# Performance work log

Measured on AMD Instinct MI355X. Metric: run time of the kernel, lower is better.

Reference implementation:

```python
import jax, jax.numpy as jnp
import numpy as np

N_NODES = 50000


def gcn_conv(x, edge_index, W, b, n):
    # PyG GCNConv: xW, add self-loops, symmetric degree normalization,
    # scatter-add messages from source (row) to target (col).
    xw = x @ W
    row, col = edge_index[0], edge_index[1]
    loops = jnp.arange(n, dtype=edge_index.dtype)
    row = jnp.concatenate([row, loops])
    col = jnp.concatenate([col, loops])
    deg = jax.ops.segment_sum(jnp.ones(row.shape[0], dtype=xw.dtype), col, num_segments=n)
    dinv = jnp.where(deg > 0, jax.lax.rsqrt(deg), 0.0)
    norm = dinv[row] * dinv[col]  # [E+N]
    out = jax.ops.segment_sum(xw[row] * norm[:, None], col, num_segments=n)
    return out + b


def setup_inputs() -> dict:
    key = jax.random.key(0)
    ks = jax.random.split(key, 5)
    n, d_in, d_h, d_out, n_edges = N_NODES, 128, 128, 4, 600000
    x = jax.random.normal(ks[0], (n, d_in), dtype=jnp.float32)
    edge_index = jax.random.randint(ks[1], (2, n_edges), 0, n, dtype=jnp.int64)
    W1 = jax.random.normal(ks[2], (d_in, d_h), dtype=jnp.float32) * (1.0 / np.sqrt(d_in))
    b1 = jnp.zeros((d_h,), dtype=jnp.float32)
    W2 = jax.random.normal(ks[3], (d_h, d_h), dtype=jnp.float32) * (1.0 / np.sqrt(d_h))
    b2 = jnp.zeros((d_h,), dtype=jnp.float32)
    Wfc = jax.random.normal(ks[4], (2 * d_h, d_out), dtype=jnp.float32) * (1.0 / np.sqrt(2 * d_h))
    bfc = jnp.zeros((d_out,), dtype=jnp.float32)
    return {"x": x, "edge_index": edge_index, "W1": W1, "b1": b1,
            "W2": W2, "b2": b2, "Wfc": Wfc, "bfc": bfc}


def reference(x, edge_index, W1, b1, W2, b2, Wfc, bfc):
    n = x.shape[0]
    # dropout is identity at inference (training=False)
    h = jax.nn.relu(gcn_conv(x, edge_index, W1, b1, n))
    h = jax.nn.relu(gcn_conv(h, edge_index, W2, b2, n))
    # edge-level gather + concat + linear classifier
    edge_x = jnp.concatenate([h[edge_index[0]], h[edge_index[1]]], axis=-1)  # [E, 2*d_h]
    edge_scores = edge_x @ Wfc + bfc  # [E, d_out]
    return jax.nn.log_softmax(edge_scores, axis=1)
```

## Files before the change

### kernel.cpp

```cpp
#include <hip/hip_runtime.h>
#include <math.h>
#include <stdint.h>

#define D 128
#define SCAN_CHUNK 2048
#define LDA 136

typedef __attribute__((ext_vector_type(8))) short v8s;
typedef __attribute__((ext_vector_type(4))) float v4f;

static __device__ __forceinline__ uint16_t f2bf(float f) {
    uint32_t u = __float_as_uint(f);
    u = (u + 0x7fff + ((u >> 16) & 1)) >> 16;
    return (uint16_t)u;
}
static __device__ __forceinline__ float bf2f(uint16_t h) { return __uint_as_float((uint32_t)h << 16); }
static __device__ __forceinline__ float bf_lo(uint32_t u) { return __uint_as_float(u << 16); }
static __device__ __forceinline__ float bf_hi(uint32_t u) { return __uint_as_float(u & 0xffff0000u); }


__global__ void count_kernel(const int* col, int* cnt, int E) {
    int e = blockIdx.x * blockDim.x + threadIdx.x;
    if (e < E) atomicAdd(&cnt[col[e]], 1);
}

__global__ __launch_bounds__(256) void scanA_kernel(const int* __restrict__ cnt,
                                                    int* __restrict__ bsum, int n) {
    __shared__ int wsum[4];
    int b = blockIdx.x, t = threadIdx.x;
    int base = b * SCAN_CHUNK;
    int s = 0;
#pragma unroll
    for (int k = 0; k < SCAN_CHUNK / 256; k++) {
        int i = base + k * 256 + t;
        if (i < n) s += cnt[i];
    }
#pragma unroll
    for (int off = 32; off > 0; off >>= 1) s += __shfl_xor(s, off, 64);
    if ((t & 63) == 0) wsum[t >> 6] = s;
    __syncthreads();
    if (t == 0) bsum[b] = wsum[0] + wsum[1] + wsum[2] + wsum[3];
}

__global__ __launch_bounds__(64) void scanB_kernel(const int* __restrict__ bsum,
                                                   int* __restrict__ bbase,
                                                   int* __restrict__ offs,
                                                   int nb, int n) {
    int t = threadIdx.x;
    int v = (t < nb) ? bsum[t] : 0;
    int inc = v;
#pragma unroll
    for (int off = 1; off < 64; off <<= 1) {
        int u = __shfl_up(inc, off, 64);
        if (t >= off) inc += u;
    }
    if (t < nb) bbase[t] = inc - v;
    if (t == nb - 1) offs[n] = inc;
}

__global__ __launch_bounds__(256) void scanC_kernel(const int* __restrict__ cnt,
                                                    const int* __restrict__ bbase,
                                                    int* __restrict__ offs,
                                                    float* __restrict__ dinv, int n) {
    __shared__ int stage[SCAN_CHUNK];
    __shared__ int res[SCAN_CHUNK];
    __shared__ int tsum[256];
    int b = blockIdx.x, t = threadIdx.x;
    int base = b * SCAN_CHUNK;
#pragma unroll
    for (int k = 0; k < SCAN_CHUNK / 256; k++) {
        int i = base + k * 256 + t;
        int c = (i < n) ? cnt[i] : 0;
        stage[k * 256 + t] = c;
        if (i < n) dinv[i] = rsqrtf((float)c + 1.0f);
    }
    __syncthreads();
    int my = 0;
#pragma unroll
    for (int j = 0; j < 8; j++) my += stage[t * 8 + j];
    tsum[t] = my;
    __syncthreads();
    for (int off = 1; off < 256; off <<= 1) {
        int v = (t >= off) ? tsum[t - off] : 0;
        __syncthreads();
        tsum[t] += v;
        __syncthreads();
    }
    int run = tsum[t] - my + bbase[b];
#pragma unroll
    for (int j = 0; j < 8; j++) {
        res[t * 8 + j] = run;
        run += stage[t * 8 + j];
    }
    __syncthreads();
#pragma unroll
    for (int k = 0; k < SCAN_CHUNK / 256; k++) {
        int i = base + k * 256 + t;
        if (i < n) offs[i] = res[k * 256 + t];
    }
}

__global__ void fill_kernel(const int* row, const int* col, const int* offs,
                            int* curs, int* adj, int E) {
    int e = blockIdx.x * blockDim.x + threadIdx.x;
    if (e < E) {
        int c = col[e];
        int p = atomicAdd(&curs[c], 1);
        adj[offs[c] + p] = row[e];
    }
}


__global__ __launch_bounds__(256) void packw_kernel(const float* __restrict__ W1,
                                                    const float* __restrict__ W2,
                                                    uint16_t* __restrict__ Wh,
                                                    uint16_t* __restrict__ Wl) {
    int i = blockIdx.x * blockDim.x + threadIdx.x;
    int layer = i >> 14;
    int li = i & 16383;
    int j = li & 7, lane = (li >> 3) & 63, f = li >> 9;
    int kstep = f >> 3, tile = f & 7;
    int k = kstep * 32 + ((lane >> 4) * 8) + j;
    int nn = tile * 16 + (lane & 15);
    const float* W = layer ? W2 : W1;
    float v = W[k * 128 + nn];
    uint16_t h = f2bf(v);
    uint16_t l = f2bf(v - bf2f(h));
    Wh[i] = h;
    Wl[i] = l;
}


__global__ __launch_bounds__(256) void gemm_mfma_kernel(const float* __restrict__ A,
                                                        const uint16_t* __restrict__ Wph,
                                                        const uint16_t* __restrict__ Wpl,
                                                        const float* __restrict__ dinv,
                                                        uint16_t* __restrict__ Cb, int M) {
    __shared__ uint16_t Ah[64][LDA];
    __shared__ uint16_t Al[64][LDA];
    int t = threadIdx.x;
    int base_row = blockIdx.x * 64;

#pragma unroll
    for (int kk = 0; kk < 8; kk++) {
        int idx = kk * 256 + t;
        int r = idx >> 5;
        int c4 = idx & 31;
        int gr = base_row + r;
        float4 f = (gr < M) ? *(const float4*)(A + (size_t)gr * D + c4 * 4)
                            : make_float4(0.f, 0.f, 0.f, 0.f);
        uint16_t h0 = f2bf(f.x), h1 = f2bf(f.y), h2 = f2bf(f.z), h3 = f2bf(f.w);
        uint16_t l0 = f2bf(f.x - bf2f(h0)), l1 = f2bf(f.y - bf2f(h1));
        uint16_t l2 = f2bf(f.z - bf2f(h2)), l3 = f2bf(f.w - bf2f(h3));
        *(ushort4*)&Ah[r][c4 * 4] = make_ushort4(h0, h1, h2, h3);
        *(ushort4*)&Al[r][c4 * 4] = make_ushort4(l0, l1, l2, l3);
    }
    __syncthreads();

    int lane = t & 63, w = t >> 6;
    int m_l = lane & 15, quad = lane >> 4;
    int arow = w * 16 + m_l;

    v4f acc[8];
#pragma unroll
    for (int i = 0; i < 8; i++) acc[i] = (v4f){0.f, 0.f, 0.f, 0.f};

#pragma unroll
    for (int ks = 0; ks < 4; ks++) {
        v8s ah = *(const v8s*)&Ah[arow][ks * 32 + quad * 8];
        v8s al = *(const v8s*)&Al[arow][ks * 32 + quad * 8];
#pragma unroll
        for (int ti = 0; ti < 8; ti++) {
            int f = ks * 8 + ti;
            v8s bh = *(const v8s*)(Wph + ((size_t)(f * 64 + lane)) * 8);
            v8s bl = *(const v8s*)(Wpl + ((size_t)(f * 64 + lane)) * 8);
            acc[ti] = __builtin_amdgcn_mfma_f32_16x16x32_bf16(al, bh, acc[ti], 0, 0, 0);
            acc[ti] = __builtin_amdgcn_mfma_f32_16x16x32_bf16(ah, bl, acc[ti], 0, 0, 0);
            acc[ti] = __builtin_amdgcn_mfma_f32_16x16x32_bf16(ah, bh, acc[ti], 0, 0, 0);
        }
    }

    int rbase = base_row + w * 16 + quad * 4;
#pragma unroll
    for (int reg = 0; reg < 4; reg++) {
        int gr = rbase + reg;
        if (gr < M) {
            float di = dinv[gr];
#pragma unroll
            for (int ti = 0; ti < 8; ti++) {
                Cb[(size_t)gr * D + ti * 16 + m_l] = f2bf(di * acc[ti][reg]);
            }
        }
    }
}


__global__ __launch_bounds__(256) void agg_kernel(const uint32_t* __restrict__ xwb,
                                                  const int* __restrict__ adj,
                                                  const int* __restrict__ offs,
                                                  const float* __restrict__ dinv,
                                                  const float* __restrict__ bias,
                                                  float* __restrict__ hout, int n) {
    int wave = (int)((blockIdx.x * (size_t)blockDim.x + threadIdx.x) >> 6);
    int lane = threadIdx.x & 63;
    if (wave >= n) return;
    int i = wave;
    uint32_t su = xwb[(size_t)i * (D / 2) + lane];
    float acc0 = bf_lo(su);
    float acc1 = bf_hi(su);
    int s = offs[i], e = offs[i + 1];
    int j = s;
    for (; j + 3 < e; j += 4) {
        int r0 = adj[j], r1 = adj[j + 1], r2 = adj[j + 2], r3 = adj[j + 3];
        uint32_t u0 = xwb[(size_t)r0 * (D / 2) + lane];
        uint32_t u1 = xwb[(size_t)r1 * (D / 2) + lane];
        uint32_t u2 = xwb[(size_t)r2 * (D / 2) + lane];
        uint32_t u3 = xwb[(size_t)r3 * (D / 2) + lane];
        acc0 += bf_lo(u0); acc1 += bf_hi(u0);
        acc0 += bf_lo(u1); acc1 += bf_hi(u1);
        acc0 += bf_lo(u2); acc1 += bf_hi(u2);
        acc0 += bf_lo(u3); acc1 += bf_hi(u3);
    }
    for (; j < e; j++) {
        int r = adj[j];
        uint32_t u = xwb[(size_t)r * (D / 2) + lane];
        acc0 += bf_lo(u); acc1 += bf_hi(u);
    }
    float di = dinv[i];
    float2 bv = ((const float2*)bias)[lane];
    float o0 = fmaxf(fmaf(di, acc0, bv.x), 0.f);
    float o1 = fmaxf(fmaf(di, acc1, bv.y), 0.f);
    ((float2*)(hout + (size_t)i * D))[lane] = make_float2(o0, o1);
}


__global__ __launch_bounds__(256) void pq_kernel(const float* __restrict__ h,
                                                 const float* __restrict__ Wfc,
                                                 const float* __restrict__ bfc,
                                                 float* __restrict__ P1,
                                                 float* __restrict__ P2, int n) {
    int i = blockIdx.x * blockDim.x + threadIdx.x;
    if (i >= n) return;
    const float4* hr = (const float4*)(h + (size_t)i * D);
    const float4* W4 = (const float4*)Wfc;
    float p0 = bfc[0], p1 = bfc[1], p2 = bfc[2], p3 = bfc[3];
    float q0 = 0.f, q1 = 0.f, q2 = 0.f, q3 = 0.f;
#pragma unroll 8
    for (int kk = 0; kk < 32; kk++) {
        float4 f = hr[kk];
#pragma unroll
        for (int j = 0; j < 4; j++) {
            float fv = (j == 0) ? f.x : (j == 1) ? f.y : (j == 2) ? f.z : f.w;
            int k = kk * 4 + j;
            float4 w1 = W4[k];
            float4 w2 = W4[128 + k];
            p0 = fmaf(fv, w1.x, p0); p1 = fmaf(fv, w1.y, p1);
            p2 = fmaf(fv, w1.z, p2); p3 = fmaf(fv, w1.w, p3);
            q0 = fmaf(fv, w2.x, q0); q1 = fmaf(fv, w2.y, q1);
            q2 = fmaf(fv, w2.z, q2); q3 = fmaf(fv, w2.w, q3);
        }
    }
    ((float4*)P1)[i] = make_float4(p0, p1, p2, p3);
    ((float4*)P2)[i] = make_float4(q0, q1, q2, q3);
}


__global__ __launch_bounds__(256) void edge2_kernel(const int* __restrict__ row,
                                                    const int* __restrict__ col,
                                                    const float* __restrict__ P1,
                                                    const float* __restrict__ P2,
                                                    float* __restrict__ out, int E) {
    int e = blockIdx.x * blockDim.x + threadIdx.x;
    if (e >= E) return;
    int r = row[e], c = col[e];
    float4 a = ((const float4*)P1)[r];
    float4 b = ((const float4*)P2)[c];
    float sx = a.x + b.x, sy = a.y + b.y, sz = a.z + b.z, sw = a.w + b.w;
    float m = fmaxf(fmaxf(sx, sy), fmaxf(sz, sw));
    float e0 = expf(sx - m), e1 = expf(sy - m), e2 = expf(sz - m), e3 = expf(sw - m);
    float lse = m + logf(e0 + e1 + e2 + e3);
    *(float4*)(out + (size_t)e * 4) = make_float4(sx - lse, sy - lse, sz - lse, sw - lse);
}


extern "C" void kernel_launch(void* const* d_in, const int* in_sizes, int n_in,
                              void* d_out, int out_size, void* d_ws, size_t ws_size,
                              hipStream_t stream) {
    const float* x   = (const float*)d_in[0];
    const int*   ei  = (const int*)d_in[1];
    const float* W1  = (const float*)d_in[2];
    const float* b1  = (const float*)d_in[3];
    const float* W2  = (const float*)d_in[4];
    const float* b2  = (const float*)d_in[5];
    const float* Wfc = (const float*)d_in[6];
    const float* bfc = (const float*)d_in[7];
    float* out = (float*)d_out;

    int n = in_sizes[0] / D;
    int E = in_sizes[1] / 2;
    const int* row = ei;
    const int* col = ei + E;

    int nbScan = (n + SCAN_CHUNK - 1) / SCAN_CHUNK;

    uint16_t* xwb  = (uint16_t*)d_ws;
    float*    h    = (float*)(xwb + (size_t)n * D);
    int*      cnt  = (int*)(h + (size_t)n * D);
    int*      curs = cnt + n;
    int*      offs = curs + n;
    int*      bsum = offs + (n + 1);
    int*      bbase= bsum + nbScan;
    int*      adj  = bbase + nbScan;
    float*    dinv = (float*)(adj + E);
    uint16_t* Wph  = (uint16_t*)(dinv + n);
    uint16_t* Wpl  = Wph + 2 * 16384;

    int nb_n = (n + 255) / 256;
    int nb_e = (E + 255) / 256;

    packw_kernel<<<128, 256, 0, stream>>>(W1, W2, Wph, Wpl);

    hipMemsetAsync(cnt, 0, (size_t)2 * n * sizeof(int), stream);
    count_kernel<<<nb_e, 256, 0, stream>>>(col, cnt, E);
    scanA_kernel<<<nbScan, 256, 0, stream>>>(cnt, bsum, n);
    scanB_kernel<<<1, 64, 0, stream>>>(bsum, bbase, offs, nbScan, n);
    scanC_kernel<<<nbScan, 256, 0, stream>>>(cnt, bbase, offs, dinv, n);
    fill_kernel<<<nb_e, 256, 0, stream>>>(row, col, offs, curs, adj, E);

    int nbG = (n + 63) / 64;

    gemm_mfma_kernel<<<nbG, 256, 0, stream>>>(x, Wph, Wpl, dinv, xwb, n);
    agg_kernel<<<(n + 3) / 4, 256, 0, stream>>>((const uint32_t*)xwb, adj, offs, dinv, b1, h, n);
    gemm_mfma_kernel<<<nbG, 256, 0, stream>>>(h, Wph + 16384, Wpl + 16384, dinv, xwb, n);
    agg_kernel<<<(n + 3) / 4, 256, 0, stream>>>((const uint32_t*)xwb, adj, offs, dinv, b2, h, n);

    float* P1 = (float*)xwb;
    float* P2 = P1 + (size_t)n * 4;
    pq_kernel<<<nb_n, 256, 0, stream>>>(h, Wfc, bfc, P1, P2, n);
    edge2_kernel<<<nb_e, 256, 0, stream>>>(row, col, P1, P2, out, E);
}
```

Before: 270.4 us.

## Fuse pack/count, merge scan stages, widen agg gathers, fuse agg2 with classifier

Folds the weight packing into the degree-count kernel and drops the separate scanB launch by having every scanC block redo the small block-sum scan, with dinv now computed in scanA. The aggregation kernel is rewritten so each wave gathers four neighbor rows at once with 16-byte loads per lane, then reduces across quarter-waves. The second aggregation is fused with the per-node classifier projection, so h is never written and reread. The aim is fewer launches and better memory-level parallelism in the gather, at the cost of extra shuffles and redundant per-block scan work.

```diff
diff --git a/kernel.cpp b/kernel.cpp
--- a/kernel.cpp
+++ b/kernel.cpp
@@ -19,13 +19,30 @@
 static __device__ __forceinline__ float bf_hi(uint32_t u) { return __uint_as_float(u & 0xffff0000u); }
 
 
-__global__ void count_kernel(const int* col, int* cnt, int E) {
-    int e = blockIdx.x * blockDim.x + threadIdx.x;
-    if (e < E) atomicAdd(&cnt[col[e]], 1);
-}
+__global__ void countpack_kernel(const int* __restrict__ col, int* __restrict__ cnt, int E,
+                                 const float* __restrict__ W1, const float* __restrict__ W2,
+                                 uint16_t* __restrict__ Wh, uint16_t* __restrict__ Wl) {
+    int tid = blockIdx.x * blockDim.x + threadIdx.x;
+    if (tid < 2 * 16384) {
+        int layer = tid >> 14;
+        int li = tid & 16383;
+        int j = li & 7, lane = (li >> 3) & 63, f = li >> 9;
+        int kstep = f >> 3, tile = f & 7;
+        int k = kstep * 32 + ((lane >> 4) * 8) + j;
+        int nn = tile * 16 + (lane & 15);
+        const float* W = layer ? W2 : W1;
+        float v = W[k * 128 + nn];
+        uint16_t h = f2bf(v);
+        Wh[tid] = h;
+        Wl[tid] = f2bf(v - bf2f(h));
+    }
+    if (tid < E) atomicAdd(&cnt[col[tid]], 1);
+}
+
 
 __global__ __launch_bounds__(256) void scanA_kernel(const int* __restrict__ cnt,
-                                                    int* __restrict__ bsum, int n) {
+                                                    int* __restrict__ bsum,
+                                                    float* __restrict__ dinv, int n) {
     __shared__ int wsum[4];
     int b = blockIdx.x, t = threadIdx.x;
     int base = b * SCAN_CHUNK;
@@ -33,7 +50,11 @@
 #pragma unroll
     for (int k = 0; k < SCAN_CHUNK / 256; k++) {
         int i = base + k * 256 + t;
-        if (i < n) s += cnt[i];
+        if (i < n) {
+            int c = cnt[i];
+            s += c;
+            dinv[i] = rsqrtf((float)c + 1.0f);
+        }
     }
 #pragma unroll
     for (int off = 32; off > 0; off >>= 1) s += __shfl_xor(s, off, 64);
@@ -42,37 +63,30 @@
     if (t == 0) bsum[b] = wsum[0] + wsum[1] + wsum[2] + wsum[3];
 }
 
-__global__ __launch_bounds__(64) void scanB_kernel(const int* __restrict__ bsum,
-                                                   int* __restrict__ bbase,
-                                                   int* __restrict__ offs,
-                                                   int nb, int n) {
-    int t = threadIdx.x;
-    int v = (t < nb) ? bsum[t] : 0;
-    int inc = v;
-#pragma unroll
-    for (int off = 1; off < 64; off <<= 1) {
-        int u = __shfl_up(inc, off, 64);
-        if (t >= off) inc += u;
-    }
-    if (t < nb) bbase[t] = inc - v;
-    if (t == nb - 1) offs[n] = inc;
-}
 
 __global__ __launch_bounds__(256) void scanC_kernel(const int* __restrict__ cnt,
-                                                    const int* __restrict__ bbase,
-                                                    int* __restrict__ offs,
-                                                    float* __restrict__ dinv, int n) {
+                                                    const int* __restrict__ bsum,
+                                                    int* __restrict__ offs, int n, int nb) {
     __shared__ int stage[SCAN_CHUNK];
     __shared__ int res[SCAN_CHUNK];
     __shared__ int tsum[256];
+    __shared__ int sb[64];
     int b = blockIdx.x, t = threadIdx.x;
+    if (t < 64) {
+        int v = (t < nb) ? bsum[t] : 0;
+        int inc = v;
+#pragma unroll
+        for (int off = 1; off < 64; off <<= 1) {
+            int u = __shfl_up(inc, off, 64);
+            if (t >= off) inc += u;
+        }
+        sb[t] = inc;
+    }
     int base = b * SCAN_CHUNK;
 #pragma unroll
     for (int k = 0; k < SCAN_CHUNK / 256; k++) {
         int i = base + k * 256 + t;
-        int c = (i < n) ? cnt[i] : 0;
-        stage[k * 256 + t] = c;
-        if (i < n) dinv[i] = rsqrtf((float)c + 1.0f);
+        stage[k * 256 + t] = (i < n) ? cnt[i] : 0;
     }
     __syncthreads();
     int my = 0;
@@ -86,7 +100,8 @@
         tsum[t] += v;
         __syncthreads();
     }
-    int run = tsum[t] - my + bbase[b];
+    int bbase = (b == 0) ? 0 : sb[b - 1];
+    int run = tsum[t] - my + bbase;
 #pragma unroll
     for (int j = 0; j < 8; j++) {
         res[t * 8 + j] = run;
@@ -98,6 +113,7 @@
         int i = base + k * 256 + t;
         if (i < n) offs[i] = res[k * 256 + t];
     }
+    if (b == gridDim.x - 1 && t == 0) offs[n] = sb[nb - 1];
 }
 
 __global__ void fill_kernel(const int* row, const int* col, const int* offs,
@@ -108,26 +124,6 @@
         int p = atomicAdd(&curs[c], 1);
         adj[offs[c] + p] = row[e];
     }
-}
-
-
-__global__ __launch_bounds__(256) void packw_kernel(const float* __restrict__ W1,
-                                                    const float* __restrict__ W2,
-                                                    uint16_t* __restrict__ Wh,
-                                                    uint16_t* __restrict__ Wl) {
-    int i = blockIdx.x * blockDim.x + threadIdx.x;
-    int layer = i >> 14;
-    int li = i & 16383;
-    int j = li & 7, lane = (li >> 3) & 63, f = li >> 9;
-    int kstep = f >> 3, tile = f & 7;
-    int k = kstep * 32 + ((lane >> 4) * 8) + j;
-    int nn = tile * 16 + (lane & 15);
-    const float* W = layer ? W2 : W1;
-    float v = W[k * 128 + nn];
-    uint16_t h = f2bf(v);
-    uint16_t l = f2bf(v - bf2f(h));
-    Wh[i] = h;
-    Wl[i] = l;
 }
 
 
@@ -195,73 +191,121 @@
 }
 
 
-__global__ __launch_bounds__(256) void agg_kernel(const uint32_t* __restrict__ xwb,
-                                                  const int* __restrict__ adj,
-                                                  const int* __restrict__ offs,
-                                                  const float* __restrict__ dinv,
-                                                  const float* __restrict__ bias,
-                                                  float* __restrict__ hout, int n) {
+#define AGG_GATHER(ACC_STMT)                                                     \
+    int s = offs[i], e = offs[i + 1];                                            \
+    int total = e - s + 1;                                                       \
+    float a0=0,a1=0,a2=0,a3=0,a4=0,a5=0,a6=0,a7=0;                               \
+    const uint4* xw4 = (const uint4*)xwb;                                        \
+    int vt = 0;                                                                  \
+    for (; vt + 8 <= total; vt += 8) {                                           \
+        int m0 = vt + q, m1 = vt + 4 + q;                                        \
+        int r0 = (m0 > 0) ? adj[s + m0 - 1] : i;                                 \
+        int r1 = adj[s + m1 - 1];                                                \
+        uint4 u0 = xw4[(size_t)r0 * 16 + sl];                                    \
+        uint4 u1 = xw4[(size_t)r1 * 16 + sl];                                    \
+        { uint4 u = u0; ACC_STMT }                                               \
+        { uint4 u = u1; ACC_STMT }                                               \
+    }                                                                            \
+    for (; vt < total; vt += 4) {                                                \
+        int myv = vt + q;                                                        \
+        bool valid = myv < total;                                                \
+        int r = i;                                                               \
+        if (valid && myv > 0) r = adj[s + myv - 1];                              \
+        uint4 u = xw4[(size_t)r * 16 + sl];                                      \
+        if (valid) { ACC_STMT }                                                  \
+    }                                                                            \
+    a0 += __shfl_xor(a0, 16, 64); a1 += __shfl_xor(a1, 16, 64);                  \
+    a2 += __shfl_xor(a2, 16, 64); a3 += __shfl_xor(a3, 16, 64);                  \
+    a4 += __shfl_xor(a4, 16, 64); a5 += __shfl_xor(a5, 16, 64);                  \
+    a6 += __shfl_xor(a6, 16, 64); a7 += __shfl_xor(a7, 16, 64);                  \
+    a0 += __shfl_xor(a0, 32, 64); a1 += __shfl_xor(a1, 32, 64);                  \
+    a2 += __shfl_xor(a2, 32, 64); a3 += __shfl_xor(a3, 32, 64);                  \
+    a4 += __shfl_xor(a4, 32, 64); a5 += __shfl_xor(a5, 32, 64);                  \
+    a6 += __shfl_xor(a6, 32, 64); a7 += __shfl_xor(a7, 32, 64);
+
+#define ACC8 \
+    a0 += bf_lo(u.x); a1 += bf_hi(u.x); a2 += bf_lo(u.y); a3 += bf_hi(u.y); \
+    a4 += bf_lo(u.z); a5 += bf_hi(u.z); a6 += bf_lo(u.w); a7 += bf_hi(u.w);
+
+__global__ __launch_bounds__(256) void agg1_kernel(const uint32_t* __restrict__ xwb,
+                                                   const int* __restrict__ adj,
+                                                   const int* __restrict__ offs,
+                                                   const float* __restrict__ dinv,
+                                                   const float* __restrict__ bias,
+                                                   float* __restrict__ hout, int n) {
     int wave = (int)((blockIdx.x * (size_t)blockDim.x + threadIdx.x) >> 6);
+    if (wave >= n) return;
     int lane = threadIdx.x & 63;
+    int q = lane >> 4, sl = lane & 15;
+    int i = wave;
+    AGG_GATHER(ACC8)
+    if (q == 0) {
+        float di = dinv[i];
+        float4 b0 = ((const float4*)bias)[2 * sl];
+        float4 b1 = ((const float4*)bias)[2 * sl + 1];
+        float4 o0, o1;
+        o0.x = fmaxf(fmaf(di, a0, b0.x), 0.f);
+        o0.y = fmaxf(fmaf(di, a1, b0.y), 0.f);
+        o0.z = fmaxf(fmaf(di, a2, b0.z), 0.f);
+        o0.w = fmaxf(fmaf(di, a3, b0.w), 0.f);
+        o1.x = fmaxf(fmaf(di, a4, b1.x), 0.f);
+        o1.y = fmaxf(fmaf(di, a5, b1.y), 0.f);
+        o1.z = fmaxf(fmaf(di, a6, b1.z), 0.f);
+        o1.w = fmaxf(fmaf(di, a7, b1.w), 0.f);
+        ((float4*)(hout + (size_t)i * D))[2 * sl] = o0;
+        ((float4*)(hout + (size_t)i * D))[2 * sl + 1] = o1;
+    }
+}
+
+__global__ __launch_bounds__(256) void agg2pq_kernel(const uint32_t* __restrict__ xwb,
+                                                     const int* __restrict__ adj,
+                                                     const int* __restrict__ offs,
+                                                     const float* __restrict__ dinv,
+                                                     const float* __restrict__ bias,
+                                                     const float* __restrict__ Wfc,
+                                                     const float* __restrict__ bfc,
+                                                     float* __restrict__ P1,
+                                                     float* __restrict__ P2, int n) {
+    int wave = (int)((blockIdx.x * (size_t)blockDim.x + threadIdx.x) >> 6);
     if (wave >= n) return;
+    int lane = threadIdx.x & 63;
+    int q = lane >> 4, sl = lane & 15;
     int i = wave;
-    uint32_t su = xwb[(size_t)i * (D / 2) + lane];
-    float acc0 = bf_lo(su);
-    float acc1 = bf_hi(su);
-    int s = offs[i], e = offs[i + 1];
-    int j = s;
-    for (; j + 3 < e; j += 4) {
-        int r0 = adj[j], r1 = adj[j + 1], r2 = adj[j + 2], r3 = adj[j + 3];
-        uint32_t u0 = xwb[(size_t)r0 * (D / 2) + lane];
-        uint32_t u1 = xwb[(size_t)r1 * (D / 2) + lane];
-        uint32_t u2 = xwb[(size_t)r2 * (D / 2) + lane];
-        uint32_t u3 = xwb[(size_t)r3 * (D / 2) + lane];
-        acc0 += bf_lo(u0); acc1 += bf_hi(u0);
-        acc0 += bf_lo(u1); acc1 += bf_hi(u1);
-        acc0 += bf_lo(u2); acc1 += bf_hi(u2);
-        acc0 += bf_lo(u3); acc1 += bf_hi(u3);
-    }
-    for (; j < e; j++) {
-        int r = adj[j];
-        uint32_t u = xwb[(size_t)r * (D / 2) + lane];
-        acc0 += bf_lo(u); acc1 += bf_hi(u);
-    }
+    AGG_GATHER(ACC8)
     float di = dinv[i];
-    float2 bv = ((const float2*)bias)[lane];
-    float o0 = fmaxf(fmaf(di, acc0, bv.x), 0.f);
-    float o1 = fmaxf(fmaf(di, acc1, bv.y), 0.f);
-    ((float2*)(hout + (size_t)i * D))[lane] = make_float2(o0, o1);
-}
-
-
-__global__ __launch_bounds__(256) void pq_kernel(const float* __restrict__ h,
-                                                 const float* __restrict__ Wfc,
-                                                 const float* __restrict__ bfc,
-                                                 float* __restrict__ P1,
-                                                 float* __restrict__ P2, int n) {
-    int i = blockIdx.x * blockDim.x + threadIdx.x;
-    if (i >= n) return;
-    const float4* hr = (const float4*)(h + (size_t)i * D);
+    float4 b0 = ((const float4*)bias)[2 * sl];
+    float4 b1 = ((const float4*)bias)[2 * sl + 1];
+    float o[8];
+    o[0] = fmaxf(fmaf(di, a0, b0.x), 0.f);
+    o[1] = fmaxf(fmaf(di, a1, b0.y), 0.f);
+    o[2] = fmaxf(fmaf(di, a2, b0.z), 0.f);
+    o[3] = fmaxf(fmaf(di, a3, b0.w), 0.f);
+    o[4] = fmaxf(fmaf(di, a4, b1.x), 0.f);
+    o[5] = fmaxf(fmaf(di, a5, b1.y), 0.f);
+    o[6] = fmaxf(fmaf(di, a6, b1.z), 0.f);
+    o[7] = fmaxf(fmaf(di, a7, b1.w), 0.f);
+    float p[8] = {0.f, 0.f, 0.f, 0.f, 0.f, 0.f, 0.f, 0.f};
     const float4* W4 = (const float4*)Wfc;
-    float p0 = bfc[0], p1 = bfc[1], p2 = bfc[2], p3 = bfc[3];
-    float q0 = 0.f, q1 = 0.f, q2 = 0.f, q3 = 0.f;
-#pragma unroll 8
-    for (int kk = 0; kk < 32; kk++) {
-        float4 f = hr[kk];
-#pragma unroll
-        for (int j = 0; j < 4; j++) {
-            float fv = (j == 0) ? f.x : (j == 1) ? f.y : (j == 2) ? f.z : f.w;
-            int k = kk * 4 + j;
-            float4 w1 = W4[k];
-            float4 w2 = W4[128 + k];
-            p0 = fmaf(fv, w1.x, p0); p1 = fmaf(fv, w1.y, p1);
-            p2 = fmaf(fv, w1.z, p2); p3 = fmaf(fv, w1.w, p3);
-            q0 = fmaf(fv, w2.x, q0); q1 = fmaf(fv, w2.y, q1);
-            q2 = fmaf(fv, w2.z, q2); q3 = fmaf(fv, w2.w, q3);
-        }
-    }
-    ((float4*)P1)[i] = make_float4(p0, p1, p2, p3);
-    ((float4*)P2)[i] = make_float4(q0, q1, q2, q3);
+#pragma unroll
+    for (int tt = 0; tt < 8; tt++) {
+        int f = 8 * sl + tt;
+        float4 w1 = W4[f];
+        float4 w2 = W4[128 + f];
+        p[0] = fmaf(o[tt], w1.x, p[0]); p[1] = fmaf(o[tt], w1.y, p[1]);
+        p[2] = fmaf(o[tt], w1.z, p[2]); p[3] = fmaf(o[tt], w1.w, p[3]);
+        p[4] = fmaf(o[tt], w2.x, p[4]); p[5] = fmaf(o[tt], w2.y, p[5]);
+        p[6] = fmaf(o[tt], w2.z, p[6]); p[7] = fmaf(o[tt], w2.w, p[7]);
+    }
+#pragma unroll
+    for (int off = 1; off < 64; off <<= 1) {
+#pragma unroll
+        for (int j = 0; j < 8; j++) p[j] += __shfl_xor(p[j], off, 64);
+    }
+    if (lane == 0) {
+        ((float4*)P1)[i] = make_float4(0.25f * p[0] + bfc[0], 0.25f * p[1] + bfc[1],
+                                       0.25f * p[2] + bfc[2], 0.25f * p[3] + bfc[3]);
+        ((float4*)P2)[i] = make_float4(0.25f * p[4], 0.25f * p[5], 0.25f * p[6], 0.25f * p[7]);
+    }
 }
 
 
@@ -308,34 +352,28 @@
     int*      cnt  = (int*)(h + (size_t)n * D);
     int*      curs = cnt + n;
     int*      offs = curs + n;
-    int*      bsum = offs + (n + 1);
-    int*      bbase= bsum + nbScan;
-    int*      adj  = bbase + nbScan;
+    int*      bsum = offs + (n + 4);
+    int*      adj  = bsum + 64;
     float*    dinv = (float*)(adj + E);
     uint16_t* Wph  = (uint16_t*)(dinv + n);
     uint16_t* Wpl  = Wph + 2 * 16384;
-
-    int nb_n = (n + 255) / 256;
+    float*    P1   = (float*)(Wpl + 2 * 16384);
+    float*    P2   = P1 + (size_t)n * 4;
+
     int nb_e = (E + 255) / 256;
 
-    packw_kernel<<<128, 256, 0, stream>>>(W1, W2, Wph, Wpl);
-
     hipMemsetAsync(cnt, 0, (size_t)2 * n * sizeof(int), stream);
-    count_kernel<<<nb_e, 256, 0, stream>>>(col, cnt, E);
-    scanA_kernel<<<nbScan, 256, 0, stream>>>(cnt, bsum, n);
-    scanB_kernel<<<1, 64, 0, stream>>>(bsum, bbase, offs, nbScan, n);
-    scanC_kernel<<<nbScan, 256, 0, stream>>>(cnt, bbase, offs, dinv, n);
+    countpack_kernel<<<nb_e, 256, 0, stream>>>(col, cnt, E, W1, W2, Wph, Wpl);
+    scanA_kernel<<<nbScan, 256, 0, stream>>>(cnt, bsum, dinv, n);
+    scanC_kernel<<<nbScan, 256, 0, stream>>>(cnt, bsum, offs, n, nbScan);
     fill_kernel<<<nb_e, 256, 0, stream>>>(row, col, offs, curs, adj, E);
 
     int nbG = (n + 63) / 64;
 
     gemm_mfma_kernel<<<nbG, 256, 0, stream>>>(x, Wph, Wpl, dinv, xwb, n);
-    agg_kernel<<<(n + 3) / 4, 256, 0, stream>>>((const uint32_t*)xwb, adj, offs, dinv, b1, h, n);
+    agg1_kernel<<<(n + 3) / 4, 256, 0, stream>>>((const uint32_t*)xwb, adj, offs, dinv, b1, h, n);
     gemm_mfma_kernel<<<nbG, 256, 0, stream>>>(h, Wph + 16384, Wpl + 16384, dinv, xwb, n);
-    agg_kernel<<<(n + 3) / 4, 256, 0, stream>>>((const uint32_t*)xwb, adj, offs, dinv, b2, h, n);
-
-    float* P1 = (float*)xwb;
-    float* P2 = P1 + (size_t)n * 4;
-    pq_kernel<<<nb_n, 256, 0, stream>>>(h, Wfc, bfc, P1, P2, n);
+    agg2pq_kernel<<<(n + 3) / 4, 256, 0, stream>>>((const uint32_t*)xwb, adj, offs, dinv, b2,
+                                                   Wfc, bfc, P1, P2, n);
     edge2_kernel<<<nb_e, 256, 0, stream>>>(row, col, P1, P2, out, E);
 }
```

Result: slower. 323.3 us (+19.6%).
